# Performance work log

Hardware: AMD Instinct MI355X
Metric: run time of the kernel (lower is better)

## Reference

```python
import jax, jax.numpy as jnp
import numpy as np

B, T, J, D_IN = 16, 128, 75, 3
HID, OUT, E = 64, 256, 300


def setup_inputs() -> dict:
    key = jax.random.key(0)
    ks = jax.random.split(key, 6)
    x = jax.random.normal(ks[0], (B, T, J, D_IN), dtype=jnp.float32)
    edge_index = jax.random.randint(ks[1], (2, E), 0, J, dtype=jnp.int64)
    W1 = jax.random.normal(ks[2], (D_IN, HID), dtype=jnp.float32) * (1.0 / np.sqrt(D_IN))
    b1 = jax.random.normal(ks[3], (HID,), dtype=jnp.float32) * 0.02
    W2 = jax.random.normal(ks[4], (HID, OUT), dtype=jnp.float32) * (1.0 / np.sqrt(HID))
    b2 = jax.random.normal(ks[5], (OUT,), dtype=jnp.float32) * 0.02
    return {"x": x, "edge_index": edge_index, "W1": W1, "b1": b1, "W2": W2, "b2": b2}


def _gcn_norm(edge_index, num_nodes, dtype):
    # PyG gcn_norm: add self-loops, norm = deg^{-1/2}[src] * deg^{-1/2}[dst]
    loops = jnp.arange(num_nodes, dtype=edge_index.dtype)
    src = jnp.concatenate([edge_index[0], loops])
    dst = jnp.concatenate([edge_index[1], loops])
    deg = jnp.zeros((num_nodes,), dtype).at[dst].add(jnp.ones_like(dst, dtype))
    dis = jax.lax.rsqrt(deg)  # deg >= 1 due to self loops
    norm = dis[src] * dis[dst]  # (E+J,)
    return src, dst, norm


def _gcn_layer(h, W, b, src, dst, norm):
    # h: (BT, J, Din) -> (BT, J, Dout). Linear first, then normalized scatter-add.
    h = h @ W
    msgs = h[:, src, :] * norm[None, :, None]        # (BT, E+J, Dout)
    agg = jnp.zeros_like(h).at[:, dst, :].add(msgs)  # (BT, J, Dout)
    return agg + b


def reference(x, edge_index, W1, b1, W2, b2):
    Bx, Tx, Jx, Dx = x.shape
    h = x.reshape(Bx * Tx, Jx, Dx)
    src, dst, norm = _gcn_norm(edge_index, Jx, x.dtype)
    h = jax.nn.gelu(_gcn_layer(h, W1, b1, src, dst, norm), approximate=False)
    h = jax.nn.gelu(_gcn_layer(h, W2, b2, src, dst, norm), approximate=False)
    return h.reshape(Bx, Tx, Jx, -1)
```

## Files before the change

### kernel.cpp

```cpp
#include <hip/hip_runtime.h>
#include <hip/hip_bf16.h>
#include <math.h>

#define J 75
#define EDGES 300
#define MAXE (EDGES + J)
#define HID 64
#define OUTF 256
#define BT 2048
#define MTOT (BT * J)
#define K2_BM 128
#define K2_BLOCKS (MTOT / K2_BM)
#define BSPW 66
#define BSPROWS 96
#define CSTR2 72

typedef __attribute__((ext_vector_type(8))) short short8;
typedef __attribute__((ext_vector_type(4))) float f32x4;

__device__ __forceinline__ unsigned short f32_to_bf16_rn(float f) {
    unsigned u = __float_as_uint(f);
    unsigned r = u + 0x7FFFu + ((u >> 16) & 1u);
    return (unsigned short)(r >> 16);
}
__device__ __forceinline__ float bf16_to_f32(unsigned short h) {
    return __uint_as_float(((unsigned)h) << 16);
}
__device__ __forceinline__ float gelu_fast(float v) {
    float v2 = v * v;
    float t  = fmaf(v2, 0.044715f, 1.0f);
    float z  = 0.7978845608028654f * v * t;
    float e  = __expf(2.0f * z);
    float r  = __builtin_amdgcn_rcpf(e + 1.0f);
    return v * (1.0f - r);
}

__global__ void prep_kernel(const int* __restrict__ ei,
                            const float* __restrict__ W2,
                            int* __restrict__ csr_off,
                            unsigned short* __restrict__ csr_src,
                            float* __restrict__ csr_norm,
                            unsigned short* __restrict__ Whi,
                            unsigned short* __restrict__ Wlo,
                            unsigned short* __restrict__ Ahi,
                            unsigned short* __restrict__ Alo) {
    const int tid = threadIdx.x;

    if (blockIdx.x < 64) {
        int t = blockIdx.x * 256 + tid;
        int j    = t & 7;
        int lane = (t >> 3) & 63;
        int nt   = (t >> 9) & 15;
        int kc   = t >> 13;
        int k = kc * 32 + (lane >> 4) * 8 + j;
        int n = nt * 16 + (lane & 15);
        float w = W2[k * OUTF + n];
        unsigned short hi = f32_to_bf16_rn(w);
        Whi[t] = hi;
        Wlo[t] = f32_to_bf16_rn(w - bf16_to_f32(hi));
        return;
    }

    if (blockIdx.x == 64) {
        __shared__ int   deg[J];
        __shared__ int   off[J + 1];
        __shared__ int   cur[J];
        __shared__ float dis[J];
        if (tid < J) { deg[tid] = 1; cur[tid] = 0; }
        __syncthreads();
        for (int e = tid; e < EDGES; e += 256) atomicAdd(&deg[ei[EDGES + e]], 1);
        __syncthreads();
        if (tid == 0) {
            int s = 0;
            for (int j = 0; j < J; ++j) { off[j] = s; s += deg[j]; }
            off[J] = s;
        }
        if (tid < J) dis[tid] = rsqrtf((float)deg[tid]);
        __syncthreads();
        for (int e = tid; e < EDGES; e += 256) {
            int s = ei[e], d = ei[EDGES + e];
            int p = off[d] + atomicAdd(&cur[d], 1);
            csr_src[p]  = (unsigned short)s;
            csr_norm[p] = dis[s] * dis[d];
        }
        for (int j = tid; j < J; j += 256) {
            int p = off[j] + atomicAdd(&cur[j], 1);
            csr_src[p]  = (unsigned short)j;
            csr_norm[p] = dis[j] * dis[j];
        }
        __syncthreads();
        for (int j = tid; j <= J; j += 256) csr_off[j] = off[j];
        return;
    }

    __shared__ float Ad[80 * 96];
    __shared__ int   deg2[J];
    __shared__ float dis2[J];
    for (int i = tid; i < 80 * 96; i += 256) Ad[i] = 0.f;
    if (tid < J) deg2[tid] = 1;
    __syncthreads();
    for (int e = tid; e < EDGES; e += 256) atomicAdd(&deg2[ei[EDGES + e]], 1);
    __syncthreads();
    if (tid < J) dis2[tid] = rsqrtf((float)deg2[tid]);
    __syncthreads();
    for (int e = tid; e < EDGES; e += 256) {
        int s = ei[e], d = ei[EDGES + e];
        atomicAdd(&Ad[d * 96 + s], dis2[s] * dis2[d]);
    }
    __syncthreads();
    if (tid < J) Ad[tid * 96 + tid] += dis2[tid] * dis2[tid];
    __syncthreads();
    for (int t = tid; t < 15 * 512; t += 256) {
        int jj   = t & 7;
        int lane = (t >> 3) & 63;
        int f    = t >> 9;
        int mt = f / 3, kc = f - mt * 3;
        int m = mt * 16 + (lane & 15);
        int k = kc * 32 + (lane >> 4) * 8 + jj;
        float v = Ad[m * 96 + k];
        unsigned short hi = f32_to_bf16_rn(v);
        Ahi[t] = hi;
        Alo[t] = f32_to_bf16_rn(v - bf16_to_f32(hi));
    }
}

__global__ void __launch_bounds__(256, 4) gcn_l1_kernel(
        const float* __restrict__ xg,
        const float* __restrict__ W1,
        const float* __restrict__ b1,
        const int*   __restrict__ csr_off,
        const unsigned short* __restrict__ csr_src,
        const float* __restrict__ csr_norm,
        const unsigned short* __restrict__ Ahi,
        const unsigned short* __restrict__ Alo,
        unsigned short* __restrict__ Chi,
        unsigned short* __restrict__ Clo) {
    __shared__ __align__(16) unsigned int Bsp[BSPROWS * BSPW];
    __shared__ float xs[J * 3];
    __shared__ float ax[J * 3];
    __shared__ float W1s[3 * HID];
    __shared__ float b1s[HID];
    __shared__ int   offs[J + 1];
    __shared__ unsigned short srcs[MAXE];
    __shared__ float nrms[MAXE];

    const int tid  = threadIdx.x;
    const int bt   = blockIdx.x;
    const int wv   = tid >> 6;
    const int lane = tid & 63;
    const int quad = lane >> 4;
    const int l16  = lane & 15;

    if (tid < J + 1) offs[tid] = csr_off[tid];
    for (int i = tid; i < MAXE; i += 256) { srcs[i] = csr_src[i]; nrms[i] = csr_norm[i]; }
    if (tid < 3 * HID) W1s[tid] = W1[tid];
    if (tid < HID)     b1s[tid] = b1[tid];
    for (int i = tid; i < J * 3; i += 256) xs[i] = xg[bt * (J * 3) + i];
    __syncthreads();

    for (int idx = tid; idx < J * 3; idx += 256) {
        int j = idx / 3, d = idx - j * 3;
        float s = 0.f;
        int p0 = offs[j], p1 = offs[j + 1];
        for (int p = p0; p < p1; ++p) s += nrms[p] * xs[srcs[p] * 3 + d];
        ax[idx] = s;
    }
    __syncthreads();

    for (int idx = tid; idx < J * HID; idx += 256) {
        int j = idx >> 6, f = idx & 63;
        float v = ax[j * 3 + 0] * W1s[0 * HID + f]
                + ax[j * 3 + 1] * W1s[1 * HID + f]
                + ax[j * 3 + 2] * W1s[2 * HID + f]
                + b1s[f];
        float g = gelu_fast(v);
        unsigned short hi = f32_to_bf16_rn(g);
        unsigned short lo = f32_to_bf16_rn(g - bf16_to_f32(hi));
        Bsp[j * BSPW + f] = (unsigned)hi | ((unsigned)lo << 16);
    }
    for (int idx = tid; idx < (BSPROWS - J) * BSPW; idx += 256) {
        int r = J + idx / BSPW, c = idx - (idx / BSPW) * BSPW;
        Bsp[r * BSPW + c] = 0u;
    }
    __syncthreads();

    f32x4 cacc[5] = {};
    const short8* Ahi8 = (const short8*)Ahi;
    const short8* Alo8 = (const short8*)Alo;
#pragma unroll
    for (int kc = 0; kc < 3; ++kc) {
        unsigned w[8];
#pragma unroll
        for (int jj = 0; jj < 8; ++jj)
            w[jj] = Bsp[(kc * 32 + quad * 8 + jj) * BSPW + wv * 16 + l16];
        short8 bh, bl;
#pragma unroll
        for (int jj = 0; jj < 8; ++jj) {
            bh[jj] = (short)(w[jj] & 0xFFFFu);
            bl[jj] = (short)(w[jj] >> 16);
        }
#pragma unroll
        for (int mt = 0; mt < 5; ++mt) {
            short8 ah = Ahi8[(mt * 3 + kc) * 64 + lane];
            short8 al = Alo8[(mt * 3 + kc) * 64 + lane];
            cacc[mt] = __builtin_amdgcn_mfma_f32_16x16x32_bf16(ah, bh, cacc[mt], 0, 0, 0);
            cacc[mt] = __builtin_amdgcn_mfma_f32_16x16x32_bf16(ah, bl, cacc[mt], 0, 0, 0);
            cacc[mt] = __builtin_amdgcn_mfma_f32_16x16x32_bf16(al, bh, cacc[mt], 0, 0, 0);
        }
    }

    const int col = wv * 16 + l16;
#pragma unroll
    for (int mt = 0; mt < 5; ++mt) {
#pragma unroll
        for (int r = 0; r < 4; ++r) {
            int row = mt * 16 + quad * 4 + r;
            if (row < J) {
                float v = cacc[mt][r];
                unsigned short hi = f32_to_bf16_rn(v);
                unsigned short lo = f32_to_bf16_rn(v - bf16_to_f32(hi));
                size_t o = (size_t)(bt * J + row) * HID + col;
                Chi[o] = hi;
                Clo[o] = lo;
            }
        }
    }
}

__global__ void __launch_bounds__(256, 4) gcn_l2_kernel(
        const unsigned short* __restrict__ Chi,
        const unsigned short* __restrict__ Clo,
        const unsigned short* __restrict__ Whi,
        const unsigned short* __restrict__ Wlo,
        const float* __restrict__ b2,
        float* __restrict__ outg) {
    const int tid  = threadIdx.x;
    const int wv   = tid >> 6;
    const int lane = tid & 63;
    const int quad = lane >> 4;
    const int l16  = lane & 15;
    const int m0   = blockIdx.x * K2_BM;

    const short8* Whi8 = (const short8*)Whi;
    const short8* Wlo8 = (const short8*)Wlo;
    const short8* CH8  = (const short8*)Chi;
    const short8* CL8  = (const short8*)Clo;

#pragma unroll
    for (int p = 0; p < 2; ++p) {
        short8 wh[2][2], wl[2][2];
        float  b2v[2];
#pragma unroll
        for (int kc = 0; kc < 2; ++kc)
#pragma unroll
            for (int q2 = 0; q2 < 2; ++q2) {
                int nt = wv * 4 + p * 2 + q2;
                int fi = (kc * 16 + nt) * 64 + lane;
                wh[kc][q2] = Whi8[fi];
                wl[kc][q2] = Wlo8[fi];
            }
#pragma unroll
        for (int q2 = 0; q2 < 2; ++q2) b2v[q2] = b2[(wv * 4 + p * 2 + q2) * 16 + l16];

        for (int mt = 0; mt < 8; ++mt) {
            size_t fbase = (size_t)(m0 + mt * 16 + l16) * 8 + quad;
            short8 ah0 = CH8[fbase + 0];
            short8 al0 = CL8[fbase + 0];
            short8 ah1 = CH8[fbase + 4];
            short8 al1 = CL8[fbase + 4];

            f32x4 acc[2];
#pragma unroll
            for (int q2 = 0; q2 < 2; ++q2)
                acc[q2] = (f32x4){b2v[q2], b2v[q2], b2v[q2], b2v[q2]};

#pragma unroll
            for (int q2 = 0; q2 < 2; ++q2) {
                acc[q2] = __builtin_amdgcn_mfma_f32_16x16x32_bf16(ah0, wh[0][q2], acc[q2], 0, 0, 0);
                acc[q2] = __builtin_amdgcn_mfma_f32_16x16x32_bf16(ah0, wl[0][q2], acc[q2], 0, 0, 0);
                acc[q2] = __builtin_amdgcn_mfma_f32_16x16x32_bf16(al0, wh[0][q2], acc[q2], 0, 0, 0);
                acc[q2] = __builtin_amdgcn_mfma_f32_16x16x32_bf16(ah1, wh[1][q2], acc[q2], 0, 0, 0);
                acc[q2] = __builtin_amdgcn_mfma_f32_16x16x32_bf16(ah1, wl[1][q2], acc[q2], 0, 0, 0);
                acc[q2] = __builtin_amdgcn_mfma_f32_16x16x32_bf16(al1, wh[1][q2], acc[q2], 0, 0, 0);
            }

#pragma unroll
            for (int q2 = 0; q2 < 2; ++q2) {
                int o = (wv * 4 + p * 2 + q2) * 16 + l16;
#pragma unroll
                for (int r = 0; r < 4; ++r) {
                    int row = m0 + mt * 16 + quad * 4 + r;
                    outg[(size_t)row * OUTF + o] = gelu_fast(acc[q2][r]);
                }
            }
        }
    }
}

__global__ void __launch_bounds__(256, 4) gcn_fused_kernel(
        const float* __restrict__ xg,
        const float* __restrict__ W1,
        const float* __restrict__ b1,
        const float* __restrict__ b2,
        const int*   __restrict__ csr_off,
        const unsigned short* __restrict__ csr_src,
        const float* __restrict__ csr_norm,
        const unsigned short* __restrict__ Whi,
        const unsigned short* __restrict__ Wlo,
        const unsigned short* __restrict__ Ahi,
        const unsigned short* __restrict__ Alo,
        float* __restrict__ outg) {
    __shared__ __align__(16) unsigned int Ubuf[BSPROWS * BSPW];
    __shared__ float xs[J * 3];
    __shared__ float ax[J * 3];
    __shared__ float W1s[3 * HID];
    __shared__ float b1s[HID];
    __shared__ float b2s[OUTF];
    __shared__ int   offs[J + 1];
    __shared__ unsigned short srcs[MAXE];
    __shared__ float nrms[MAXE];

    const int tid  = threadIdx.x;
    const int bt   = blockIdx.x;
    const int wv   = tid >> 6;
    const int lane = tid & 63;
    const int quad = lane >> 4;
    const int l16  = lane & 15;

    if (tid < J + 1) offs[tid] = csr_off[tid];
    for (int i = tid; i < MAXE; i += 256) { srcs[i] = csr_src[i]; nrms[i] = csr_norm[i]; }
    if (tid < 3 * HID) W1s[tid] = W1[tid];
    if (tid < HID)     b1s[tid] = b1[tid];
    if (tid < OUTF)    b2s[tid] = b2[tid];
    for (int i = tid; i < J * 3; i += 256) xs[i] = xg[bt * (J * 3) + i];
    __syncthreads();

    for (int idx = tid; idx < J * 3; idx += 256) {
        int j = idx / 3, d = idx - j * 3;
        float s = 0.f;
        int p0 = offs[j], p1 = offs[j + 1];
        for (int p = p0; p < p1; ++p) s += nrms[p] * xs[srcs[p] * 3 + d];
        ax[idx] = s;
    }
    __syncthreads();

    for (int idx = tid; idx < J * HID; idx += 256) {
        int j = idx >> 6, f = idx & 63;
        float v = ax[j * 3 + 0] * W1s[0 * HID + f]
                + ax[j * 3 + 1] * W1s[1 * HID + f]
                + ax[j * 3 + 2] * W1s[2 * HID + f]
                + b1s[f];
        float g = gelu_fast(v);
        unsigned short hi = f32_to_bf16_rn(g);
        unsigned short lo = f32_to_bf16_rn(g - bf16_to_f32(hi));
        Ubuf[j * BSPW + f] = (unsigned)hi | ((unsigned)lo << 16);
    }
    for (int idx = tid; idx < (BSPROWS - J) * BSPW; idx += 256) {
        int r = J + idx / BSPW, c = idx - (idx / BSPW) * BSPW;
        Ubuf[r * BSPW + c] = 0u;
    }
    __syncthreads();

    f32x4 cacc[5] = {};
    const short8* Ahi8 = (const short8*)Ahi;
    const short8* Alo8 = (const short8*)Alo;
#pragma unroll
    for (int kc = 0; kc < 3; ++kc) {
        unsigned w[8];
#pragma unroll
        for (int jj = 0; jj < 8; ++jj)
            w[jj] = Ubuf[(kc * 32 + quad * 8 + jj) * BSPW + wv * 16 + l16];
        short8 bh, bl;
#pragma unroll
        for (int jj = 0; jj < 8; ++jj) {
            bh[jj] = (short)(w[jj] & 0xFFFFu);
            bl[jj] = (short)(w[jj] >> 16);
        }
#pragma unroll
        for (int mt = 0; mt < 5; ++mt) {
            short8 ah = Ahi8[(mt * 3 + kc) * 64 + lane];
            short8 al = Alo8[(mt * 3 + kc) * 64 + lane];
            cacc[mt] = __builtin_amdgcn_mfma_f32_16x16x32_bf16(ah, bh, cacc[mt], 0, 0, 0);
            cacc[mt] = __builtin_amdgcn_mfma_f32_16x16x32_bf16(ah, bl, cacc[mt], 0, 0, 0);
            cacc[mt] = __builtin_amdgcn_mfma_f32_16x16x32_bf16(al, bh, cacc[mt], 0, 0, 0);
        }
    }
    __syncthreads();

    unsigned short* CH = (unsigned short*)Ubuf;
    unsigned short* CL = CH + 80 * CSTR2;
#pragma unroll
    for (int mt = 0; mt < 5; ++mt) {
#pragma unroll
        for (int r = 0; r < 4; ++r) {
            int node = mt * 16 + quad * 4 + r;
            int feat = wv * 16 + l16;
            float v = cacc[mt][r];
            unsigned short hi = f32_to_bf16_rn(v);
            unsigned short lo = f32_to_bf16_rn(v - bf16_to_f32(hi));
            CH[node * CSTR2 + feat] = hi;
            CL[node * CSTR2 + feat] = lo;
        }
    }
    __syncthreads();

    const short8* Whi8 = (const short8*)Whi;
    const short8* Wlo8 = (const short8*)Wlo;
    float* outb = outg + (size_t)bt * (J * OUTF);

#pragma unroll
    for (int p = 0; p < 2; ++p) {
        f32x4 acc[5][2];
#pragma unroll
        for (int q2 = 0; q2 < 2; ++q2) {
            int nt2 = wv * 4 + p * 2 + q2;
            float bv = b2s[nt2 * 16 + l16];
#pragma unroll
            for (int mt = 0; mt < 5; ++mt) acc[mt][q2] = (f32x4){bv, bv, bv, bv};
        }
#pragma unroll
        for (int kc = 0; kc < 2; ++kc) {
            short8 wh[2], wl[2];
#pragma unroll
            for (int q2 = 0; q2 < 2; ++q2) {
                int nt2 = wv * 4 + p * 2 + q2;
                int fi = (kc * 16 + nt2) * 64 + lane;
                wh[q2] = Whi8[fi];
                wl[q2] = Wlo8[fi];
            }
#pragma unroll
            for (int mt = 0; mt < 5; ++mt) {
                const unsigned short* ab = &CH[(mt * 16 + l16) * CSTR2 + kc * 32 + quad * 8];
                short8 ah = *(const short8*)ab;
                short8 al = *(const short8*)(ab + 80 * CSTR2);
#pragma unroll
                for (int q2 = 0; q2 < 2; ++q2) {
                    acc[mt][q2] = __builtin_amdgcn_mfma_f32_16x16x32_bf16(ah, wh[q2], acc[mt][q2], 0, 0, 0);
                    acc[mt][q2] = __builtin_amdgcn_mfma_f32_16x16x32_bf16(ah, wl[q2], acc[mt][q2], 0, 0, 0);
                    acc[mt][q2] = __builtin_amdgcn_mfma_f32_16x16x32_bf16(al, wh[q2], acc[mt][q2], 0, 0, 0);
                }
            }
        }
#pragma unroll
        for (int mt = 0; mt < 5; ++mt) {
#pragma unroll
            for (int q2 = 0; q2 < 2; ++q2) {
                int o = (wv * 4 + p * 2 + q2) * 16 + l16;
#pragma unroll
                for (int r = 0; r < 4; ++r) {
                    int row = mt * 16 + quad * 4 + r;
                    if (row < J)
                        outb[row * OUTF + o] = gelu_fast(acc[mt][q2][r]);
                }
            }
        }
    }
}

extern "C" void kernel_launch(void* const* d_in, const int* in_sizes, int n_in,
                              void* d_out, int out_size, void* d_ws, size_t ws_size,
                              hipStream_t stream) {
    const float* x  = (const float*)d_in[0];
    const int*   ei = (const int*)d_in[1];
    const float* W1 = (const float*)d_in[2];
    const float* b1 = (const float*)d_in[3];
    const float* W2 = (const float*)d_in[4];
    const float* b2 = (const float*)d_in[5];
    float* out = (float*)d_out;

    char* ws = (char*)d_ws;
    int*            csr_off  = (int*)ws;
    unsigned short* csr_src  = (unsigned short*)(ws + 512);
    float*          csr_norm = (float*)(ws + 2048);
    unsigned short* Whi      = (unsigned short*)(ws + 4096);
    unsigned short* Wlo      = (unsigned short*)(ws + 36864);
    unsigned short* Ahi      = (unsigned short*)(ws + 69632);
    unsigned short* Alo      = (unsigned short*)(ws + 86016);
    const size_t CPLANE = (size_t)MTOT * HID * sizeof(unsigned short);
    unsigned short* Chi      = (unsigned short*)(ws + 102400);
    unsigned short* Clo      = (unsigned short*)(ws + 102400 + CPLANE);
    const size_t need = 102400 + 2 * CPLANE;

    prep_kernel<<<66, 256, 0, stream>>>(ei, W2, csr_off, csr_src, csr_norm,
                                        Whi, Wlo, Ahi, Alo);
    if (ws_size >= need) {
        gcn_l1_kernel<<<BT, 256, 0, stream>>>(x, W1, b1,
                                              csr_off, csr_src, csr_norm,
                                              Ahi, Alo, Chi, Clo);
        gcn_l2_kernel<<<K2_BLOCKS, 256, 0, stream>>>(Chi, Clo, Whi, Wlo, b2, out);
    } else {
        gcn_fused_kernel<<<BT, 256, 0, stream>>>(x, W1, b1, b2,
                                                 csr_off, csr_src, csr_norm,
                                                 Whi, Wlo, Ahi, Alo, out);
    }
}
```

Measured before the change: 219.6 us.

## Interleave hi/lo bf16 intermediate into one buffer and widen layer-2 tile per wave

Layer 1 now writes the hi and lo bf16 halves of each hidden value packed into one 32-bit word, replacing two separate planes. Layer 2 reads them with 16-byte loads and unpacks them in registers. Layer 2 also drops the two-pass loop over output column pairs: each wave keeps all four column tiles' weights in registers and reads each A row tile only once instead of twice. This cuts repeated global reads of the intermediate at the cost of more registers per wave, which could lower occupancy.

New measurement: 227.8 us. 3.7% more time.

```diff
diff --git a/kernel.cpp b/kernel.cpp
--- a/kernel.cpp
+++ b/kernel.cpp
@@ -133,8 +133,7 @@
         const float* __restrict__ csr_norm,
         const unsigned short* __restrict__ Ahi,
         const unsigned short* __restrict__ Alo,
-        unsigned short* __restrict__ Chi,
-        unsigned short* __restrict__ Clo) {
+        unsigned int* __restrict__ Cp) {
     __shared__ __align__(16) unsigned int Bsp[BSPROWS * BSPW];
     __shared__ float xs[J * 3];
     __shared__ float ax[J * 3];
@@ -219,17 +218,14 @@
                 float v = cacc[mt][r];
                 unsigned short hi = f32_to_bf16_rn(v);
                 unsigned short lo = f32_to_bf16_rn(v - bf16_to_f32(hi));
-                size_t o = (size_t)(bt * J + row) * HID + col;
-                Chi[o] = hi;
-                Clo[o] = lo;
+                Cp[(size_t)(bt * J + row) * HID + col] = (unsigned)hi | ((unsigned)lo << 16);
             }
         }
     }
 }
 
 __global__ void __launch_bounds__(256, 4) gcn_l2_kernel(
-        const unsigned short* __restrict__ Chi,
-        const unsigned short* __restrict__ Clo,
+        const unsigned int* __restrict__ Cp,
         const unsigned short* __restrict__ Whi,
         const unsigned short* __restrict__ Wlo,
         const float* __restrict__ b2,
@@ -243,55 +239,56 @@
 
     const short8* Whi8 = (const short8*)Whi;
     const short8* Wlo8 = (const short8*)Wlo;
-    const short8* CH8  = (const short8*)Chi;
-    const short8* CL8  = (const short8*)Clo;
-
-#pragma unroll
-    for (int p = 0; p < 2; ++p) {
-        short8 wh[2][2], wl[2][2];
-        float  b2v[2];
-#pragma unroll
-        for (int kc = 0; kc < 2; ++kc)
-#pragma unroll
-            for (int q2 = 0; q2 < 2; ++q2) {
-                int nt = wv * 4 + p * 2 + q2;
-                int fi = (kc * 16 + nt) * 64 + lane;
-                wh[kc][q2] = Whi8[fi];
-                wl[kc][q2] = Wlo8[fi];
-            }
-#pragma unroll
-        for (int q2 = 0; q2 < 2; ++q2) b2v[q2] = b2[(wv * 4 + p * 2 + q2) * 16 + l16];
-
-        for (int mt = 0; mt < 8; ++mt) {
-            size_t fbase = (size_t)(m0 + mt * 16 + l16) * 8 + quad;
-            short8 ah0 = CH8[fbase + 0];
-            short8 al0 = CL8[fbase + 0];
-            short8 ah1 = CH8[fbase + 4];
-            short8 al1 = CL8[fbase + 4];
-
-            f32x4 acc[2];
-#pragma unroll
-            for (int q2 = 0; q2 < 2; ++q2)
-                acc[q2] = (f32x4){b2v[q2], b2v[q2], b2v[q2], b2v[q2]};
-
-#pragma unroll
-            for (int q2 = 0; q2 < 2; ++q2) {
-                acc[q2] = __builtin_amdgcn_mfma_f32_16x16x32_bf16(ah0, wh[0][q2], acc[q2], 0, 0, 0);
-                acc[q2] = __builtin_amdgcn_mfma_f32_16x16x32_bf16(ah0, wl[0][q2], acc[q2], 0, 0, 0);
-                acc[q2] = __builtin_amdgcn_mfma_f32_16x16x32_bf16(al0, wh[0][q2], acc[q2], 0, 0, 0);
-                acc[q2] = __builtin_amdgcn_mfma_f32_16x16x32_bf16(ah1, wh[1][q2], acc[q2], 0, 0, 0);
-                acc[q2] = __builtin_amdgcn_mfma_f32_16x16x32_bf16(ah1, wl[1][q2], acc[q2], 0, 0, 0);
-                acc[q2] = __builtin_amdgcn_mfma_f32_16x16x32_bf16(al1, wh[1][q2], acc[q2], 0, 0, 0);
-            }
-
-#pragma unroll
-            for (int q2 = 0; q2 < 2; ++q2) {
-                int o = (wv * 4 + p * 2 + q2) * 16 + l16;
-#pragma unroll
-                for (int r = 0; r < 4; ++r) {
-                    int row = m0 + mt * 16 + quad * 4 + r;
-                    outg[(size_t)row * OUTF + o] = gelu_fast(acc[q2][r]);
-                }
+
+    short8 wh[2][4], wl[2][4];
+    float  b2v[4];
+#pragma unroll
+    for (int kc = 0; kc < 2; ++kc)
+#pragma unroll
+        for (int q = 0; q < 4; ++q) {
+            int nt = wv * 4 + q;
+            int fi = (kc * 16 + nt) * 64 + lane;
+            wh[kc][q] = Whi8[fi];
+            wl[kc][q] = Wlo8[fi];
+        }
+#pragma unroll
+    for (int q = 0; q < 4; ++q) b2v[q] = b2[(wv * 4 + q) * 16 + l16];
+
+#pragma unroll 1
+    for (int mt = 0; mt < 8; ++mt) {
+        const int row = m0 + mt * 16 + l16;
+        const uint4* cr = (const uint4*)(Cp + (size_t)row * HID) + quad * 2;
+
+        f32x4 acc[4];
+#pragma unroll
+        for (int q = 0; q < 4; ++q) acc[q] = (f32x4){b2v[q], b2v[q], b2v[q], b2v[q]};
+
+#pragma unroll
+        for (int kc = 0; kc < 2; ++kc) {
+            uint4 w0 = cr[kc * 8 + 0];
+            uint4 w1 = cr[kc * 8 + 1];
+            unsigned cw[8] = {w0.x, w0.y, w0.z, w0.w, w1.x, w1.y, w1.z, w1.w};
+            short8 ah, al;
+#pragma unroll
+            for (int j = 0; j < 8; ++j) {
+                ah[j] = (short)(cw[j] & 0xFFFFu);
+                al[j] = (short)(cw[j] >> 16);
+            }
+#pragma unroll
+            for (int q = 0; q < 4; ++q) {
+                acc[q] = __builtin_amdgcn_mfma_f32_16x16x32_bf16(ah, wh[kc][q], acc[q], 0, 0, 0);
+                acc[q] = __builtin_amdgcn_mfma_f32_16x16x32_bf16(ah, wl[kc][q], acc[q], 0, 0, 0);
+                acc[q] = __builtin_amdgcn_mfma_f32_16x16x32_bf16(al, wh[kc][q], acc[q], 0, 0, 0);
+            }
+        }
+
+#pragma unroll
+        for (int q = 0; q < 4; ++q) {
+            int o = (wv * 4 + q) * 16 + l16;
+#pragma unroll
+            for (int r = 0; r < 4; ++r) {
+                int orow = m0 + mt * 16 + quad * 4 + r;
+                outg[(size_t)orow * OUTF + o] = gelu_fast(acc[q][r]);
             }
         }
     }
@@ -476,18 +473,17 @@
     unsigned short* Wlo      = (unsigned short*)(ws + 36864);
     unsigned short* Ahi      = (unsigned short*)(ws + 69632);
     unsigned short* Alo      = (unsigned short*)(ws + 86016);
-    const size_t CPLANE = (size_t)MTOT * HID * sizeof(unsigned short);
-    unsigned short* Chi      = (unsigned short*)(ws + 102400);
-    unsigned short* Clo      = (unsigned short*)(ws + 102400 + CPLANE);
-    const size_t need = 102400 + 2 * CPLANE;
+    unsigned int*   Cp       = (unsigned int*)(ws + 102400);
+    const size_t CPLANE = (size_t)MTOT * HID * sizeof(unsigned int);
+    const size_t need = 102400 + CPLANE;
 
     prep_kernel<<<66, 256, 0, stream>>>(ei, W2, csr_off, csr_src, csr_norm,
                                         Whi, Wlo, Ahi, Alo);
     if (ws_size >= need) {
         gcn_l1_kernel<<<BT, 256, 0, stream>>>(x, W1, b1,
                                               csr_off, csr_src, csr_norm,
-                                              Ahi, Alo, Chi, Clo);
-        gcn_l2_kernel<<<K2_BLOCKS, 256, 0, stream>>>(Chi, Clo, Whi, Wlo, b2, out);
+                                              Ahi, Alo, Cp);
+        gcn_l2_kernel<<<K2_BLOCKS, 256, 0, stream>>>(Cp, Whi, Wlo, b2, out);
     } else {
         gcn_fused_kernel<<<BT, 256, 0, stream>>>(x, W1, b1, b2,
                                                  csr_off, csr_src, csr_norm,
```
